# Kernel tuning notes

Measured on AMD Instinct MI355X. Metric: run time of the kernel, lower is better.

## Reference

```python
import jax, jax.numpy as jnp
import numpy as np

DIM = 192
HEADS = 4
EPS = 1e-12  # F.normalize default eps


def setup_inputs() -> dict:
    key = jax.random.key(0)
    k0, k1, k2, k3 = jax.random.split(key, 4)
    x = jax.random.normal(k0, (4, DIM, 128, 128), dtype=jnp.float32)
    # qkv 1x1 conv weight: [3*dim, dim, 1, 1] -> stored as [3*dim, dim]
    w_qkv = jax.random.normal(k1, (3 * DIM, DIM), dtype=jnp.float32) * (1.0 / np.sqrt(DIM))
    # depthwise 3x3 conv weight: [3*dim, 1, 3, 3]
    w_dw = jax.random.normal(k2, (3 * DIM, 1, 3, 3), dtype=jnp.float32) * (1.0 / 3.0)
    # project_out 1x1 conv weight: [dim, dim]
    w_proj = jax.random.normal(k3, (DIM, DIM), dtype=jnp.float32) * (1.0 / np.sqrt(DIM))
    # temperature: ones(heads,1,1), requires_grad=False in original
    temperature = jnp.ones((HEADS, 1, 1), dtype=jnp.float32)
    return {"x": x, "w_qkv": w_qkv, "w_dw": w_dw, "w_proj": w_proj,
            "temperature": temperature}


def _l2norm(t):
    # F.normalize(t, dim=-1): t / max(||t||_2, eps)
    n = jnp.sqrt(jnp.sum(t * t, axis=-1, keepdims=True))
    return t / jnp.maximum(n, EPS)


def reference(x, w_qkv, w_dw, w_proj, temperature):
    b, c, h, w = x.shape
    ch = c // HEADS  # channels per head
    # 1x1 conv (no bias) == channel GEMM
    qkv = jnp.einsum('oc,bchw->bohw', w_qkv, x)
    # depthwise 3x3 conv, padding=1, groups=3*dim
    qkv = jax.lax.conv_general_dilated(
        qkv, w_dw, window_strides=(1, 1), padding=((1, 1), (1, 1)),
        dimension_numbers=('NCHW', 'OIHW', 'NCHW'),
        feature_group_count=3 * c)
    q, k, v = jnp.split(qkv, 3, axis=1)
    # b (head ch) h w -> b head ch (h w)
    def rearr(t):
        return t.reshape(b, HEADS, ch, h * w)
    q, k, v = rearr(q), rearr(k), rearr(v)
    q = _l2norm(q)
    k = _l2norm(k)
    # channel-channel attention: [b, head, ch, ch]
    attn = jnp.einsum('bhcn,bhdn->bhcd', q, k) * temperature[None]
    attn = jax.nn.softmax(attn, axis=-1)
    out = jnp.einsum('bhcd,bhdn->bhcn', attn, v)
    out = out.reshape(b, c, h, w)
    out = jnp.einsum('oc,bchw->bohw', w_proj, out)
    return out
```

## Files before the change

kernel.cpp:

```cpp
#include <hip/hip_runtime.h>

typedef unsigned short u16;
typedef float f32x4 __attribute__((ext_vector_type(4)));
typedef __bf16 bf16x8 __attribute__((ext_vector_type(8)));
typedef unsigned short u16x8 __attribute__((ext_vector_type(8)));

#define DEV static __device__ __forceinline__

DEV u16 f2bf(float f) {
  unsigned int u = __float_as_uint(f);
  u += 0x7FFFu + ((u >> 16) & 1u);
  return (u16)(u >> 16);
}
DEV float bf2f(u16 h) { return __uint_as_float(((unsigned int)h) << 16); }

DEV void gload_lds16(const void* g, void* l) {
  __builtin_amdgcn_global_load_lds(
      (__attribute__((address_space(1))) void*)(unsigned long long)g,
      (__attribute__((address_space(3))) void*)l, 16, 0, 0);
}

__global__ __launch_bounds__(256) void convert_w_kernel(
    const float* __restrict__ in, u16* __restrict__ out, int n) {
  int i = blockIdx.x * 256 + threadIdx.x;
  if (i < n) out[i] = f2bf(in[i]);
}

__global__ __launch_bounds__(256) void transpose_f32_kernel(
    const float* __restrict__ in, u16* __restrict__ out,
    size_t inBatch, size_t outBatch, int C) {
  __shared__ u16 ls[64][66];
  const int b = blockIdx.z;
  const int c0 = blockIdx.x * 64, r0 = blockIdx.y * 64;
  const float* ip = in + (size_t)b * inBatch;
  u16* op = out + (size_t)b * outBatch;
  const int t = threadIdx.x;
  const int rr = t >> 4, cg = t & 15;
#pragma unroll
  for (int i = 0; i < 4; ++i) {
    const int r = i * 16 + rr;
    const f32x4 v = *(const f32x4*)(ip + (size_t)(r0 + r) * C + c0 + cg * 4);
    ls[r][cg * 4 + 0] = f2bf(v.x);
    ls[r][cg * 4 + 1] = f2bf(v.y);
    ls[r][cg * 4 + 2] = f2bf(v.z);
    ls[r][cg * 4 + 3] = f2bf(v.w);
  }
  __syncthreads();
  const int lane = t & 63, w = t >> 6;
#pragma unroll
  for (int i = 0; i < 16; ++i) {
    const int c = i * 4 + w;
    op[(size_t)(c0 + c) * 192 + r0 + lane] = ls[lane][c];
  }
}

__global__ __launch_bounds__(256) void transpose_u16_kernel(
    const u16* __restrict__ in, u16* __restrict__ out,
    size_t inBatch, size_t outBatch, int C) {
  __shared__ u16 ls[64][66];
  const int b = blockIdx.z;
  const int c0 = blockIdx.x * 64, r0 = blockIdx.y * 64;
  const u16* ip = in + (size_t)b * inBatch;
  u16* op = out + (size_t)b * outBatch;
  const int t = threadIdx.x;
  const int rr = t >> 3, cg = t & 7;
#pragma unroll
  for (int i = 0; i < 2; ++i) {
    const int r = i * 32 + rr;
    const u16x8 v = *(const u16x8*)(ip + (size_t)(r0 + r) * C + c0 + cg * 8);
#pragma unroll
    for (int j = 0; j < 8; ++j) ls[r][cg * 8 + j] = v[j];
  }
  __syncthreads();
  const int lane = t & 63, w = t >> 6;
#pragma unroll
  for (int i = 0; i < 16; ++i) {
    const int c = i * 4 + w;
    op[(size_t)(c0 + c) * 192 + r0 + lane] = ls[lane][c];
  }
}

template <bool OUT_BF16, int NJ>
__global__ __launch_bounds__(256, 2) void gemm_bt_kernel(
    const u16* __restrict__ A, const u16* __restrict__ B, void* __restrict__ Cv,
    size_t aBatch, size_t bBatch, size_t cBatch, int ldC, int nwg) {
  __shared__ __align__(16) char smem[73728];
  u16* sA = (u16*)smem;
  u16* sB = (u16*)(smem + 49152);
  float* sC = (float*)smem;

  const int tid = threadIdx.x, wave = tid >> 6, lane = tid & 63;
  const int p = blockIdx.x;
  const int id = (p & 7) * (nwg >> 3) + (p >> 3);
  const int j = id % NJ;
  const int tt = id / NJ;
  const int m0 = (tt & 127) * 128, j0 = j * 64, b = tt >> 7;

  const char* Ab = (const char*)(A + (size_t)b * aBatch + (size_t)m0 * 192);
  const char* Bb = (const char*)(B + (size_t)b * bBatch + (size_t)j0 * 192);

#pragma unroll
  for (int i = 0; i < 12; ++i) {
    const int c = i * 4 + wave;
    const int d = c * 1024 + lane * 16;
    const int row = d / 384, inrow = d - row * 384;
    gload_lds16(Ab + row * 384 + (inrow ^ ((row & 7) << 4)),
                (char*)sA + c * 1024);
  }
#pragma unroll
  for (int i = 0; i < 6; ++i) {
    const int c = i * 4 + wave;
    const int d = c * 1024 + lane * 16;
    const int row = d / 384, inrow = d - row * 384;
    gload_lds16(Bb + row * 384 + (inrow ^ ((row & 7) << 4)),
                (char*)sB + c * 1024);
  }
  asm volatile("s_waitcnt vmcnt(0)" ::: "memory");
  __syncthreads();

  const int wm = wave & 1, wn = wave >> 1;
  const int l15 = lane & 15, lg = lane >> 4;
  const int swm = (l15 & 7) << 4;
  const int rA0 = (wm * 64 + l15) * 384, rB0 = (wn * 32 + l15) * 384;

  f32x4 acc[4][2];
#pragma unroll
  for (int mi = 0; mi < 4; ++mi)
#pragma unroll
    for (int nj = 0; nj < 2; ++nj) acc[mi][nj] = (f32x4){0.f, 0.f, 0.f, 0.f};

#pragma unroll
  for (int ks = 0; ks < 6; ++ks) {
    const int col = (ks * 64 + lg * 16) ^ swm;
    bf16x8 af[4], bfv[2];
#pragma unroll
    for (int mi = 0; mi < 4; ++mi)
      af[mi] = *(const bf16x8*)((char*)sA + rA0 + mi * 16 * 384 + col);
#pragma unroll
    for (int nj = 0; nj < 2; ++nj)
      bfv[nj] = *(const bf16x8*)((char*)sB + rB0 + nj * 16 * 384 + col);
#pragma unroll
    for (int mi = 0; mi < 4; ++mi)
#pragma unroll
      for (int nj = 0; nj < 2; ++nj)
        acc[mi][nj] = __builtin_amdgcn_mfma_f32_16x16x32_bf16(
            af[mi], bfv[nj], acc[mi][nj], 0, 0, 0);
  }
  __syncthreads();

#pragma unroll
  for (int mi = 0; mi < 4; ++mi)
#pragma unroll
    for (int nj = 0; nj < 2; ++nj)
#pragma unroll
      for (int r = 0; r < 4; ++r)
        sC[(wn * 32 + nj * 16 + l15) * 129 + (wm * 64 + mi * 16 + lg * 4 + r)] =
            acc[mi][nj][r];
  __syncthreads();
  if (OUT_BF16) {
    u16* Cb = (u16*)Cv + (size_t)b * cBatch;
#pragma unroll
    for (int i = 0; i < 32; ++i) {
      const int flat = i * 256 + tid;
      const int jj = flat >> 7, mm = flat & 127;
      Cb[(size_t)(j0 + jj) * ldC + m0 + mm] = f2bf(sC[jj * 129 + mm]);
    }
  } else {
    float* Cb = (float*)Cv + (size_t)b * cBatch;
#pragma unroll
    for (int i = 0; i < 32; ++i) {
      const int flat = i * 256 + tid;
      const int jj = flat >> 7, mm = flat & 127;
      Cb[(size_t)(j0 + jj) * ldC + m0 + mm] = sC[jj * 129 + mm];
    }
  }
}

__global__ __launch_bounds__(256) void dwconv_kernel(
    u16* __restrict__ qkv, const float* __restrict__ wdw,
    float* __restrict__ sq) {
  __shared__ u16 img[16384];
  __shared__ float red[4];
  const int o = blockIdx.x, b = blockIdx.y;
  const size_t base = ((size_t)b * 576 + o) * 16384;
  const int tid = threadIdx.x, wave = tid >> 6, lane = tid & 63;
#pragma unroll
  for (int i = 0; i < 8; ++i) {
    const int off = (i * 4 + wave) * 1024;
    gload_lds16((const char*)qkv + base * 2 + off + lane * 16, (char*)img + off);
  }
  asm volatile("s_waitcnt vmcnt(0)" ::: "memory");
  __syncthreads();
  float w[9];
#pragma unroll
  for (int j = 0; j < 9; ++j) w[j] = wdw[o * 9 + j];
  float sqacc = 0.f;
  for (int it = 0; it < 8; ++it) {
    const int chunk = it * 256 + tid;
    const int px0 = chunk * 8;
    const int y = px0 >> 7, x0 = px0 & 127;
    float acc[8];
#pragma unroll
    for (int j = 0; j < 8; ++j) acc[j] = 0.f;
#pragma unroll
    for (int dy = -1; dy <= 1; ++dy) {
      const int yy = y + dy;
      float v[10];
      if (yy >= 0 && yy <= 127) {
        const u16* rowp = img + yy * 128 + x0;
        u16x8 m = *(const u16x8*)rowp;
#pragma unroll
        for (int j = 0; j < 8; ++j) v[j + 1] = bf2f(m[j]);
        v[0] = (x0 > 0) ? bf2f(rowp[-1]) : 0.f;
        v[9] = (x0 < 120) ? bf2f(rowp[8]) : 0.f;
      } else {
#pragma unroll
        for (int j = 0; j < 10; ++j) v[j] = 0.f;
      }
      const float w0 = w[(dy + 1) * 3], w1 = w[(dy + 1) * 3 + 1],
                  w2 = w[(dy + 1) * 3 + 2];
#pragma unroll
      for (int j = 0; j < 8; ++j) acc[j] += w0 * v[j] + w1 * v[j + 1] + w2 * v[j + 2];
    }
    u16x8 ov;
#pragma unroll
    for (int j = 0; j < 8; ++j) {
      sqacc += acc[j] * acc[j];
      ov[j] = f2bf(acc[j]);
    }
    *(u16x8*)(qkv + base + px0) = ov;
  }
#pragma unroll
  for (int s = 32; s > 0; s >>= 1) sqacc += __shfl_xor(sqacc, s, 64);
  if (lane == 0) red[wave] = sqacc;
  __syncthreads();
  if (tid == 0) sq[b * 576 + o] = red[0] + red[1] + red[2] + red[3];
}

__global__ __launch_bounds__(256) void gram_kernel(
    const u16* __restrict__ qkv, float* __restrict__ partial) {
  __shared__ u16 tiles[4 * 3072];
  __shared__ float red[4 * 2304];
  const int bh = blockIdx.y, b = bh >> 2, h = bh & 3;
  const int g = blockIdx.x;
  const int wave = threadIdx.x >> 6, lane = threadIdx.x & 63;
  const int n0 = g * 1024 + wave * 256;
  const u16* qb = qkv + ((size_t)b * 576 + h * 48) * 16384;
  const u16* kb = qb + (size_t)192 * 16384;
  u16* tl = tiles + wave * 3072;
  f32x4 acc[3][3];
#pragma unroll
  for (int i = 0; i < 3; ++i)
#pragma unroll
    for (int j = 0; j < 3; ++j) acc[i][j] = (f32x4){0.f, 0.f, 0.f, 0.f};

  for (int ks = 0; ks < 8; ++ks) {
    const int nn = n0 + ks * 32;
    asm volatile("s_waitcnt lgkmcnt(0)" ::: "memory");
#pragma unroll
    for (int i = 0; i < 6; ++i) {
      const int flat = i * 1024 + lane * 16;
      const int row = flat >> 6, colb = flat & 63;
      const u16* src = (row < 48) ? (qb + (size_t)row * 16384 + nn)
                                  : (kb + (size_t)(row - 48) * 16384 + nn);
      gload_lds16((const char*)src + colb, (char*)tl + i * 1024);
    }
    asm volatile("s_waitcnt vmcnt(0)" ::: "memory");
    const int l15 = lane & 15, lg = lane >> 4;
    bf16x8 qf[3], kf[3];
#pragma unroll
    for (int f = 0; f < 3; ++f) {
      qf[f] = *(const bf16x8*)(tl + (f * 16 + l15) * 32 + lg * 8);
      kf[f] = *(const bf16x8*)(tl + (48 + f * 16 + l15) * 32 + lg * 8);
    }
#pragma unroll
    for (int i = 0; i < 3; ++i)
#pragma unroll
      for (int j = 0; j < 3; ++j)
        acc[i][j] = __builtin_amdgcn_mfma_f32_16x16x32_bf16(qf[i], kf[j],
                                                            acc[i][j], 0, 0, 0);
  }
  {
    const int l15 = lane & 15, lg = lane >> 4;
    float* rw = red + wave * 2304;
#pragma unroll
    for (int i = 0; i < 3; ++i)
#pragma unroll
      for (int j = 0; j < 3; ++j)
#pragma unroll
        for (int r = 0; r < 4; ++r)
          rw[(i * 16 + lg * 4 + r) * 48 + (j * 16 + l15)] = acc[i][j][r];
  }
  __syncthreads();
#pragma unroll
  for (int it = 0; it < 9; ++it) {
    const int p = it * 256 + threadIdx.x;
    const float s = red[p] + red[2304 + p] + red[4608 + p] + red[6912 + p];
    partial[((size_t)bh * 2304 + p) * 16 + g] = s;
  }
}

__global__ __launch_bounds__(256) void softmax_weff_kernel(
    const float* __restrict__ partial, const float* __restrict__ sq,
    const float* __restrict__ temp, const float* __restrict__ wproj,
    u16* __restrict__ weff) {
  __shared__ float G[2304];
  __shared__ float wp[192 * 49];
  __shared__ float nq[48], nk[48];
  const int bh = blockIdx.x, b = bh >> 2, h = bh & 3;
  const int tid = threadIdx.x;
#pragma unroll
  for (int it = 0; it < 36; ++it) {
    const int j = it * 256 + tid;
    const int o = j / 48, c = j - o * 48;
    wp[o * 49 + c] = wproj[o * 192 + h * 48 + c];
  }
#pragma unroll
  for (int it = 0; it < 9; ++it) {
    const int p = it * 256 + tid;
    const f32x4* pp = (const f32x4*)(partial + ((size_t)bh * 2304 + p) * 16);
    const f32x4 a = pp[0] + pp[1] + pp[2] + pp[3];
    G[p] = a.x + a.y + a.z + a.w;
  }
  if (tid < 48) {
    nq[tid] = fmaxf(sqrtf(sq[b * 576 + h * 48 + tid]), 1e-12f);
    nk[tid] = fmaxf(sqrtf(sq[b * 576 + 192 + h * 48 + tid]), 1e-12f);
  }
  __syncthreads();
  if (tid < 48) {
    const int r = tid;
    const float inq = temp[h] / nq[r];
    float L[48];
    float mx = -3.4e38f;
#pragma unroll 4
    for (int d = 0; d < 48; ++d) {
      const float v = G[r * 48 + d] * inq / nk[d];
      L[d] = v;
      mx = fmaxf(mx, v);
    }
    float s = 0.f;
#pragma unroll 4
    for (int d = 0; d < 48; ++d) {
      const float e = __expf(L[d] - mx);
      L[d] = e;
      s += e;
    }
    const float inv = 1.f / s;
#pragma unroll 4
    for (int d = 0; d < 48; ++d) G[r * 48 + d] = L[d] * inv;
  }
  __syncthreads();
  if (tid < 192) {
    const int o = tid;
    f32x4 acc[12];
#pragma unroll
    for (int dv = 0; dv < 12; ++dv) acc[dv] = (f32x4){0.f, 0.f, 0.f, 0.f};
    for (int c = 0; c < 48; ++c) {
      const float w = wp[o * 49 + c];
      const f32x4* at = (const f32x4*)(G + c * 48);
#pragma unroll
      for (int dv = 0; dv < 12; ++dv) acc[dv] += w * at[dv];
    }
    u16* op = weff + ((size_t)b * 192 + o) * 192 + h * 48;
#pragma unroll
    for (int g8 = 0; g8 < 6; ++g8) {
      u16x8 ov;
#pragma unroll
      for (int j = 0; j < 8; ++j) {
        const int d = g8 * 8 + j;
        ov[j] = f2bf(acc[d >> 2][d & 3]);
      }
      *(u16x8*)(op + g8 * 8) = ov;
    }
  }
}

extern "C" void kernel_launch(void* const* d_in, const int* in_sizes, int n_in,
                              void* d_out, int out_size, void* d_ws,
                              size_t ws_size, hipStream_t stream) {
  (void)in_sizes; (void)n_in; (void)out_size; (void)ws_size;
  const float* x      = (const float*)d_in[0];
  const float* w_qkv  = (const float*)d_in[1];
  const float* w_dw   = (const float*)d_in[2];
  const float* w_proj = (const float*)d_in[3];
  const float* temp   = (const float*)d_in[4];

  char* ws = (char*)d_ws;
  u16*   qkv     = (u16*)ws;
  u16*   vT      = (u16*)(ws + 75497472);
  float* partial = (float*)(ws + 100663296);
  float* sq      = (float*)(ws + 103022592);
  u16*   Wq      = (u16*)(ws + 103031808);
  u16*   Weff    = (u16*)(ws + 103252992);
  u16*   Xt      = (u16*)d_out;

  convert_w_kernel<<<dim3(432), 256, 0, stream>>>(w_qkv, Wq, 110592);
  transpose_f32_kernel<<<dim3(256, 3, 4), 256, 0, stream>>>(
      x, Xt, (size_t)192 * 16384, (size_t)16384 * 192, 16384);
  gemm_bt_kernel<true, 9><<<dim3(4608), 256, 0, stream>>>(
      Xt, Wq, qkv, (size_t)16384 * 192, 0, (size_t)576 * 16384, 16384, 4608);
  dwconv_kernel<<<dim3(576, 4), 256, 0, stream>>>(qkv, w_dw, sq);
  gram_kernel<<<dim3(16, 16), 256, 0, stream>>>(qkv, partial);
  softmax_weff_kernel<<<dim3(16), 256, 0, stream>>>(partial, sq, temp, w_proj,
                                                    Weff);
  transpose_u16_kernel<<<dim3(256, 3, 4), 256, 0, stream>>>(
      qkv + (size_t)384 * 16384, vT, (size_t)576 * 16384, (size_t)16384 * 192,
      16384);
  gemm_bt_kernel<false, 3><<<dim3(1536), 256, 0, stream>>>(
      vT, Weff, d_out, (size_t)16384 * 192, (size_t)192 * 192,
      (size_t)192 * 16384, 16384, 1536);
}
```

Measured before the change: 143.0 us.

## Keep A tile resident in registers and loop over N tiles per workgroup

The GEMM kernel now loads each 128-row A tile once into LDS and registers. It then iterates over all NJ column tiles of B inside one workgroup, prefetching the next B tile into LDS while the MFMAs run. Output is written directly from accumulators as vectorized stores instead of being staged through LDS. The gram kernel adds an XOR swizzle to its LDS tiles to reduce bank conflicts. The trade-offs are fewer workgroups (512), less parallelism, higher register pressure, and stores with a strided row pattern.

```diff
diff --git a/kernel.cpp b/kernel.cpp
--- a/kernel.cpp
+++ b/kernel.cpp
@@ -4,6 +4,7 @@
 typedef float f32x4 __attribute__((ext_vector_type(4)));
 typedef __bf16 bf16x8 __attribute__((ext_vector_type(8)));
 typedef unsigned short u16x8 __attribute__((ext_vector_type(8)));
+typedef unsigned short u16x4 __attribute__((ext_vector_type(4)));
 
 #define DEV static __device__ __forceinline__
 
@@ -83,95 +84,133 @@
 template <bool OUT_BF16, int NJ>
 __global__ __launch_bounds__(256, 2) void gemm_bt_kernel(
     const u16* __restrict__ A, const u16* __restrict__ B, void* __restrict__ Cv,
-    size_t aBatch, size_t bBatch, size_t cBatch, int ldC, int nwg) {
+    size_t aBatch, size_t bBatch, size_t cBatch, int ldC) {
   __shared__ __align__(16) char smem[73728];
-  u16* sA = (u16*)smem;
-  u16* sB = (u16*)(smem + 49152);
-  float* sC = (float*)smem;
+  char* sA = smem;
+  char* sB = smem + 49152;
 
   const int tid = threadIdx.x, wave = tid >> 6, lane = tid & 63;
-  const int p = blockIdx.x;
-  const int id = (p & 7) * (nwg >> 3) + (p >> 3);
-  const int j = id % NJ;
-  const int tt = id / NJ;
-  const int m0 = (tt & 127) * 128, j0 = j * 64, b = tt >> 7;
-
+  const int id = blockIdx.x;
+  const int m0 = (id & 127) * 128, b = id >> 7;
   const char* Ab = (const char*)(A + (size_t)b * aBatch + (size_t)m0 * 192);
-  const char* Bb = (const char*)(B + (size_t)b * bBatch + (size_t)j0 * 192);
+  const char* Bbase = (const char*)(B + (size_t)b * bBatch);
 
 #pragma unroll
   for (int i = 0; i < 12; ++i) {
     const int c = i * 4 + wave;
     const int d = c * 1024 + lane * 16;
     const int row = d / 384, inrow = d - row * 384;
-    gload_lds16(Ab + row * 384 + (inrow ^ ((row & 7) << 4)),
-                (char*)sA + c * 1024);
+    gload_lds16(Ab + row * 384 + (inrow ^ ((row & 7) << 4)), sA + c * 1024);
   }
 #pragma unroll
   for (int i = 0; i < 6; ++i) {
     const int c = i * 4 + wave;
     const int d = c * 1024 + lane * 16;
     const int row = d / 384, inrow = d - row * 384;
-    gload_lds16(Bb + row * 384 + (inrow ^ ((row & 7) << 4)),
-                (char*)sB + c * 1024);
+    gload_lds16(Bbase + row * 384 + (inrow ^ ((row & 7) << 4)), sB + c * 1024);
   }
   asm volatile("s_waitcnt vmcnt(0)" ::: "memory");
-  __syncthreads();
+  __builtin_amdgcn_s_barrier();
 
   const int wm = wave & 1, wn = wave >> 1;
   const int l15 = lane & 15, lg = lane >> 4;
   const int swm = (l15 & 7) << 4;
-  const int rA0 = (wm * 64 + l15) * 384, rB0 = (wn * 32 + l15) * 384;
+  const int rA0 = (wm * 64 + l15) * 384;
+  const int rB0 = (wn * 32 + l15) * 384;
+
+  bf16x8 af[4][6];
+#pragma unroll
+  for (int mi = 0; mi < 4; ++mi)
+#pragma unroll
+    for (int ks = 0; ks < 6; ++ks)
+      af[mi][ks] = *(const bf16x8*)(sA + rA0 + mi * 16 * 384 +
+                                    ((ks * 64 + lg * 16) ^ swm));
 
   f32x4 acc[4][2];
-#pragma unroll
-  for (int mi = 0; mi < 4; ++mi)
-#pragma unroll
-    for (int nj = 0; nj < 2; ++nj) acc[mi][nj] = (f32x4){0.f, 0.f, 0.f, 0.f};
-
-#pragma unroll
-  for (int ks = 0; ks < 6; ++ks) {
-    const int col = (ks * 64 + lg * 16) ^ swm;
-    bf16x8 af[4], bfv[2];
+  for (int j = 0; j < NJ; ++j) {
+    if (j > 0) {
+      const int j0 = (j - 1) * 64;
+      if (OUT_BF16) {
+        u16* Cb = (u16*)Cv + (size_t)b * cBatch;
+#pragma unroll
+        for (int mi = 0; mi < 4; ++mi)
+#pragma unroll
+          for (int nj = 0; nj < 2; ++nj) {
+            u16x4 ov;
+#pragma unroll
+            for (int r = 0; r < 4; ++r) ov[r] = f2bf(acc[mi][nj][r]);
+            *(u16x4*)(Cb + (size_t)(j0 + wn * 32 + nj * 16 + l15) * ldC + m0 +
+                      wm * 64 + mi * 16 + lg * 4) = ov;
+          }
+      } else {
+        float* Cb = (float*)Cv + (size_t)b * cBatch;
+#pragma unroll
+        for (int mi = 0; mi < 4; ++mi)
+#pragma unroll
+          for (int nj = 0; nj < 2; ++nj)
+            *(f32x4*)(Cb + (size_t)(j0 + wn * 32 + nj * 16 + l15) * ldC + m0 +
+                      wm * 64 + mi * 16 + lg * 4) = acc[mi][nj];
+      }
+    }
+    bf16x8 bfv[2][6];
+#pragma unroll
+    for (int nj = 0; nj < 2; ++nj)
+#pragma unroll
+      for (int ks = 0; ks < 6; ++ks)
+        bfv[nj][ks] = *(const bf16x8*)(sB + rB0 + nj * 16 * 384 +
+                                       ((ks * 64 + lg * 16) ^ swm));
+    asm volatile("s_waitcnt lgkmcnt(0)" ::: "memory");
+    __builtin_amdgcn_s_barrier();
+    if (j + 1 < NJ) {
+      const char* Bj = Bbase + (size_t)(j + 1) * 64 * 384;
+#pragma unroll
+      for (int i = 0; i < 6; ++i) {
+        const int c = i * 4 + wave;
+        const int d = c * 1024 + lane * 16;
+        const int row = d / 384, inrow = d - row * 384;
+        gload_lds16(Bj + row * 384 + (inrow ^ ((row & 7) << 4)), sB + c * 1024);
+      }
+    }
+    __builtin_amdgcn_sched_barrier(0);
 #pragma unroll
     for (int mi = 0; mi < 4; ++mi)
-      af[mi] = *(const bf16x8*)((char*)sA + rA0 + mi * 16 * 384 + col);
-#pragma unroll
-    for (int nj = 0; nj < 2; ++nj)
-      bfv[nj] = *(const bf16x8*)((char*)sB + rB0 + nj * 16 * 384 + col);
-#pragma unroll
-    for (int mi = 0; mi < 4; ++mi)
-#pragma unroll
-      for (int nj = 0; nj < 2; ++nj)
-        acc[mi][nj] = __builtin_amdgcn_mfma_f32_16x16x32_bf16(
-            af[mi], bfv[nj], acc[mi][nj], 0, 0, 0);
-  }
-  __syncthreads();
-
-#pragma unroll
-  for (int mi = 0; mi < 4; ++mi)
-#pragma unroll
-    for (int nj = 0; nj < 2; ++nj)
-#pragma unroll
-      for (int r = 0; r < 4; ++r)
-        sC[(wn * 32 + nj * 16 + l15) * 129 + (wm * 64 + mi * 16 + lg * 4 + r)] =
-            acc[mi][nj][r];
-  __syncthreads();
-  if (OUT_BF16) {
-    u16* Cb = (u16*)Cv + (size_t)b * cBatch;
-#pragma unroll
-    for (int i = 0; i < 32; ++i) {
-      const int flat = i * 256 + tid;
-      const int jj = flat >> 7, mm = flat & 127;
-      Cb[(size_t)(j0 + jj) * ldC + m0 + mm] = f2bf(sC[jj * 129 + mm]);
-    }
-  } else {
-    float* Cb = (float*)Cv + (size_t)b * cBatch;
-#pragma unroll
-    for (int i = 0; i < 32; ++i) {
-      const int flat = i * 256 + tid;
-      const int jj = flat >> 7, mm = flat & 127;
-      Cb[(size_t)(j0 + jj) * ldC + m0 + mm] = sC[jj * 129 + mm];
+#pragma unroll
+      for (int nj = 0; nj < 2; ++nj) acc[mi][nj] = (f32x4){0.f, 0.f, 0.f, 0.f};
+#pragma unroll
+    for (int ks = 0; ks < 6; ++ks)
+#pragma unroll
+      for (int mi = 0; mi < 4; ++mi)
+#pragma unroll
+        for (int nj = 0; nj < 2; ++nj)
+          acc[mi][nj] = __builtin_amdgcn_mfma_f32_16x16x32_bf16(
+              af[mi][ks], bfv[nj][ks], acc[mi][nj], 0, 0, 0);
+    if (j + 1 < NJ) {
+      asm volatile("s_waitcnt vmcnt(0)" ::: "memory");
+      __builtin_amdgcn_s_barrier();
+    }
+  }
+  {
+    const int j0 = (NJ - 1) * 64;
+    if (OUT_BF16) {
+      u16* Cb = (u16*)Cv + (size_t)b * cBatch;
+#pragma unroll
+      for (int mi = 0; mi < 4; ++mi)
+#pragma unroll
+        for (int nj = 0; nj < 2; ++nj) {
+          u16x4 ov;
+#pragma unroll
+          for (int r = 0; r < 4; ++r) ov[r] = f2bf(acc[mi][nj][r]);
+          *(u16x4*)(Cb + (size_t)(j0 + wn * 32 + nj * 16 + l15) * ldC + m0 +
+                    wm * 64 + mi * 16 + lg * 4) = ov;
+        }
+    } else {
+      float* Cb = (float*)Cv + (size_t)b * cBatch;
+#pragma unroll
+      for (int mi = 0; mi < 4; ++mi)
+#pragma unroll
+        for (int nj = 0; nj < 2; ++nj)
+          *(f32x4*)(Cb + (size_t)(j0 + wn * 32 + nj * 16 + l15) * ldC + m0 +
+                    wm * 64 + mi * 16 + lg * 4) = acc[mi][nj];
     }
   }
 }
@@ -247,7 +286,9 @@
   const int n0 = g * 1024 + wave * 256;
   const u16* qb = qkv + ((size_t)b * 576 + h * 48) * 16384;
   const u16* kb = qb + (size_t)192 * 16384;
-  u16* tl = tiles + wave * 3072;
+  char* tl = (char*)(tiles + wave * 3072);
+  const int l15 = lane & 15, lg = lane >> 4;
+  const int swz = (l15 & 3) << 4;
   f32x4 acc[3][3];
 #pragma unroll
   for (int i = 0; i < 3; ++i)
@@ -263,15 +304,14 @@
       const int row = flat >> 6, colb = flat & 63;
       const u16* src = (row < 48) ? (qb + (size_t)row * 16384 + nn)
                                   : (kb + (size_t)(row - 48) * 16384 + nn);
-      gload_lds16((const char*)src + colb, (char*)tl + i * 1024);
+      gload_lds16((const char*)src + (colb ^ ((row & 3) << 4)), tl + i * 1024);
     }
     asm volatile("s_waitcnt vmcnt(0)" ::: "memory");
-    const int l15 = lane & 15, lg = lane >> 4;
     bf16x8 qf[3], kf[3];
 #pragma unroll
     for (int f = 0; f < 3; ++f) {
-      qf[f] = *(const bf16x8*)(tl + (f * 16 + l15) * 32 + lg * 8);
-      kf[f] = *(const bf16x8*)(tl + (48 + f * 16 + l15) * 32 + lg * 8);
+      qf[f] = *(const bf16x8*)(tl + (f * 16 + l15) * 64 + ((lg * 16) ^ swz));
+      kf[f] = *(const bf16x8*)(tl + (48 + f * 16 + l15) * 64 + ((lg * 16) ^ swz));
     }
 #pragma unroll
     for (int i = 0; i < 3; ++i)
@@ -281,7 +321,6 @@
                                                             acc[i][j], 0, 0, 0);
   }
   {
-    const int l15 = lane & 15, lg = lane >> 4;
     float* rw = red + wave * 2304;
 #pragma unroll
     for (int i = 0; i < 3; ++i)
@@ -397,8 +436,8 @@
   convert_w_kernel<<<dim3(432), 256, 0, stream>>>(w_qkv, Wq, 110592);
   transpose_f32_kernel<<<dim3(256, 3, 4), 256, 0, stream>>>(
       x, Xt, (size_t)192 * 16384, (size_t)16384 * 192, 16384);
-  gemm_bt_kernel<true, 9><<<dim3(4608), 256, 0, stream>>>(
-      Xt, Wq, qkv, (size_t)16384 * 192, 0, (size_t)576 * 16384, 16384, 4608);
+  gemm_bt_kernel<true, 9><<<dim3(512), 256, 0, stream>>>(
+      Xt, Wq, qkv, (size_t)16384 * 192, 0, (size_t)576 * 16384, 16384);
   dwconv_kernel<<<dim3(576, 4), 256, 0, stream>>>(qkv, w_dw, sq);
   gram_kernel<<<dim3(16, 16), 256, 0, stream>>>(qkv, partial);
   softmax_weff_kernel<<<dim3(16), 256, 0, stream>>>(partial, sq, temp, w_proj,
@@ -406,7 +445,7 @@
   transpose_u16_kernel<<<dim3(256, 3, 4), 256, 0, stream>>>(
       qkv + (size_t)384 * 16384, vT, (size_t)576 * 16384, (size_t)16384 * 192,
       16384);
-  gemm_bt_kernel<false, 3><<<dim3(1536), 256, 0, stream>>>(
+  gemm_bt_kernel<false, 3><<<dim3(512), 256, 0, stream>>>(
       vT, Weff, d_out, (size_t)16384 * 192, (size_t)192 * 192,
-      (size_t)192 * 16384, 16384, 1536);
-}
+      (size_t)192 * 16384, 16384);
+}
```

After: 138.8 us. -2.9%, faster.
